# Performance work log

Hardware: AMD Instinct MI355X
Metric: run time of the kernel (lower is better)

Reference implementation:

```python
import jax, jax.numpy as jnp
import numpy as np

GAMMA = 2.0
CONTEXT_WINDOW = 100


def setup_inputs() -> dict:
    key = jax.random.key(0)
    k1, k2 = jax.random.split(key)
    B, S, C = 64, 131072, 3
    inputs = jax.random.normal(k1, (B, S, C), dtype=jnp.float32)
    targets = jax.random.randint(k2, (B, S), 0, C, dtype=jnp.int32)
    alpha = jnp.array([0.25, 1.0, 1.0], dtype=jnp.float32)
    return {"inputs": inputs, "targets": targets, "alpha": alpha}


def _window_mask(targets, window):
    # mask[b, i] = True iff any positive target within +/- window of i;
    # rows with no positives are fully True (matches torch loop semantics).
    B, S = targets.shape
    pos = targets > 0                                   # (B, S) bool
    cs = jnp.cumsum(pos.astype(jnp.int32), axis=1)      # inclusive prefix sums
    c = jnp.concatenate([jnp.zeros((B, 1), jnp.int32), cs], axis=1)  # (B, S+1)
    idx = jnp.arange(S)
    hi = jnp.minimum(idx + window + 1, S)               # exclusive end
    lo = jnp.maximum(idx - window, 0)                   # inclusive start
    count = c[:, hi] - c[:, lo]                         # positives in window
    mask = count > 0
    has_pos = pos.any(axis=1, keepdims=True)
    return jnp.where(has_pos, mask, True)


def reference(inputs, targets, alpha):
    # inputs: (B, S, C) logits; targets: (B, S) class indices
    mask = _window_mask(targets, CONTEXT_WINDOW)                     # (B, S)
    logp = jax.nn.log_softmax(inputs, axis=-1)                       # (B, S, C)
    ce = -jnp.take_along_axis(logp, targets[..., None].astype(jnp.int32), axis=-1)[..., 0]
    p_t = jnp.exp(-ce)
    focal = alpha[targets] * (1.0 - p_t) ** GAMMA * ce               # (B, S)
    m = mask.astype(inputs.dtype)
    # masked mean == mean over selected elements in the torch version
    return jnp.sum(focal * m) / jnp.sum(m)
```

## Files before the change

kernel.cpp:

```cpp
#include <hip/hip_runtime.h>

#define BB 64
#define SS 131072
#define WIN 100
#define TILE 2048
#define NTHREADS 256
#define NBLOCKS (BB * (SS / TILE))
#define EXT (TILE + 2*WIN)
#define NITER ((EXT + NTHREADS - 1) / NTHREADS)
#define NWORDS ((EXT + 63) / 64)

__global__ __launch_bounds__(NTHREADS) void focal_main(
    const float* __restrict__ inputs, const int* __restrict__ targets,
    const float* __restrict__ alpha, double* __restrict__ slots)
{
    __shared__ unsigned char sh_t[EXT];
    __shared__ unsigned long long wbits[NWORDS];
    __shared__ unsigned long long mbits[NWORDS];
    __shared__ double red[(NTHREADS/64) * 4];

    const int t = threadIdx.x;
    const int b = blockIdx.x >> 6;
    const int tile = blockIdx.x & 63;
    const int s0 = tile * TILE;
    const int ext_lo = (s0 - WIN > 0) ? (s0 - WIN) : 0;
    const int ext_hi = (s0 + TILE + WIN < SS) ? (s0 + TILE + WIN) : SS;
    const int ext_len = ext_hi - ext_lo;

    const float* inrow = inputs + (long)b * SS * 3;
    const int p0 = s0 + t * 4;
    const int p1 = s0 + (NTHREADS + t) * 4;
    const float4* ip0 = (const float4*)(inrow + (long)p0 * 3);
    const float4* ip1 = (const float4*)(inrow + (long)p1 * 3);
    const float4 q0 = ip0[0], q1 = ip0[1], q2 = ip0[2];
    const float4 q3 = ip1[0], q4 = ip1[1], q5 = ip1[2];

    const int* trow = targets + (long)b * SS;
    const int wave = t >> 6, lane = t & 63;
    const int tr_lo = s0 - ext_lo;
    int cnt_p = 0;
    #pragma unroll
    for (int it = 0; it < NITER; ++it) {
        const int k = it * NTHREADS + t;
        const int tv = (k < ext_len) ? trow[ext_lo + k] : 0;
        if (k < ext_len) sh_t[k] = (unsigned char)tv;
        const bool pos = (tv > 0);
        cnt_p += (pos && k >= tr_lo && k < tr_lo + TILE) ? 1 : 0;
        const unsigned long long bal = __ballot(pos);
        if (lane == 0) wbits[it * 4 + wave] = bal;
    }
    __syncthreads();

    if (wave == 0) {
        unsigned long long x = (lane < NWORDS) ? wbits[lane] : 0ULL;
        const int shifts[7] = {1, 2, 4, 8, 16, 32, 37};
        #pragma unroll
        for (int s_i = 0; s_i < 7; ++s_i) {
            const int s = shifts[s_i];
            unsigned long long up = __shfl_up(x, 1);
            if (lane == 0) up = 0ULL;
            unsigned long long dn = __shfl_down(x, 1);
            if (lane == 63) dn = 0ULL;
            x = x | (x << s) | (up >> (64 - s)) | (x >> s) | (dn << (64 - s));
        }
        if (lane < NWORDS) mbits[lane] = x;
    }
    __syncthreads();

    const float a0 = alpha[0], a1 = alpha[1], a2 = alpha[2];
    float fsum_m = 0.0f, fsum_a = 0.0f;
    int cnt_m = 0;

    const float xs[24] = {q0.x, q0.y, q0.z, q0.w, q1.x, q1.y, q1.z, q1.w,
                          q2.x, q2.y, q2.z, q2.w, q3.x, q3.y, q3.z, q3.w,
                          q4.x, q4.y, q4.z, q4.w, q5.x, q5.y, q5.z, q5.w};

    #pragma unroll
    for (int g = 0; g < 2; ++g) {
        const int p = (g == 0) ? p0 : p1;
        const int j0 = p - ext_lo;
        const unsigned long long mw = mbits[j0 >> 6];
        const unsigned int tpack = *(const unsigned int*)(sh_t + j0);
        #pragma unroll
        for (int j = 0; j < 4; ++j) {
            const float x0 = xs[g*12 + 3*j], x1 = xs[g*12 + 3*j + 1],
                        x2 = xs[g*12 + 3*j + 2];
            const int tv = (tpack >> (8 * j)) & 0xFF;
            const float mx = fmaxf(x0, fmaxf(x1, x2));
            const float e0 = __expf(x0 - mx), e1 = __expf(x1 - mx), e2 = __expf(x2 - mx);
            const float sum = e0 + e1 + e2;
            const float xt  = (tv == 0) ? x0 : ((tv == 1) ? x1 : x2);
            const float et  = (tv == 0) ? e0 : ((tv == 1) ? e1 : e2);
            const float ce  = __logf(sum) + (mx - xt);
            const float pt  = et * __frcp_rn(sum);
            const float w   = (tv == 0) ? a0 : ((tv == 1) ? a1 : a2);
            const float om  = 1.0f - pt;
            const float focal = w * om * om * ce;
            const bool  m   = (mw >> ((j0 & 63) + j)) & 1ULL;

            fsum_a += focal;
            fsum_m += m ? focal : 0.0f;
            cnt_m  += m ? 1 : 0;
        }
    }

    #pragma unroll
    for (int off = 32; off >= 1; off >>= 1) {
        fsum_m += __shfl_down(fsum_m, off);
        fsum_a += __shfl_down(fsum_a, off);
        cnt_m  += __shfl_down(cnt_m, off);
        cnt_p  += __shfl_down(cnt_p, off);
    }
    if (lane == 0) {
        red[wave*4]   = (double)fsum_m; red[wave*4+1] = (double)cnt_m;
        red[wave*4+2] = (double)fsum_a; red[wave*4+3] = (double)cnt_p;
    }
    __syncthreads();
    if (t == 0) {
        double sm = 0, sc = 0, sa = 0, sp = 0;
        #pragma unroll
        for (int w = 0; w < NTHREADS/64; ++w) {
            sm += red[w*4]; sc += red[w*4+1]; sa += red[w*4+2]; sp += red[w*4+3];
        }
        double* slot = slots + (long)blockIdx.x * 4;
        slot[0] = sm;
        slot[1] = sc;
        slot[2] = sa;
        slot[3] = sp;
    }
}

__global__ __launch_bounds__(NTHREADS) void focal_final(
    const double* __restrict__ slots, float* __restrict__ out)
{
    __shared__ double red[(NTHREADS/64) * 2];
    __shared__ double tot[2];
    const int t = threadIdx.x;
    const int wave = t >> 6, lane = t & 63;

    double sm = 0.0, sc = 0.0;
    for (int k = t; k < NBLOCKS; k += NTHREADS) {
        sm += slots[(long)k * 4 + 0];
        sc += slots[(long)k * 4 + 1];
    }
    #pragma unroll
    for (int off = 32; off >= 1; off >>= 1) {
        sm += __shfl_down(sm, off);
        sc += __shfl_down(sc, off);
    }
    if (lane == 0) { red[wave*2] = sm; red[wave*2+1] = sc; }
    __syncthreads();
    if (t == 0) {
        double a = 0, b = 0;
        #pragma unroll
        for (int w = 0; w < NTHREADS/64; ++w) { a += red[w*2]; b += red[w*2+1]; }
        tot[0] = a; tot[1] = b;
    }
    __syncthreads();

    double corr_s = 0.0, corr_c = 0.0;
    if (t < BB) {
        double row_sum = 0.0, row_pos = 0.0;
        for (int j = 0; j < 64; ++j) {
            const long blk = (long)t * 64 + j;
            row_sum += slots[blk * 4 + 2];
            row_pos += slots[blk * 4 + 3];
        }
        if (row_pos == 0.0) { corr_s = row_sum; corr_c = (double)SS; }
    }
    if (wave == 0) {
        #pragma unroll
        for (int off = 32; off >= 1; off >>= 1) {
            corr_s += __shfl_down(corr_s, off);
            corr_c += __shfl_down(corr_c, off);
        }
        if (t == 0) {
            const double total = tot[0] + corr_s;
            const double count = tot[1] + corr_c;
            out[0] = (float)(total / count);
        }
    }
}

extern "C" void kernel_launch(void* const* d_in, const int* in_sizes, int n_in,
                              void* d_out, int out_size, void* d_ws, size_t ws_size,
                              hipStream_t stream) {
    const float* inputs  = (const float*)d_in[0];
    const int*   targets = (const int*)d_in[1];
    const float* alpha   = (const float*)d_in[2];
    float* out = (float*)d_out;

    double* slots = (double*)d_ws;

    focal_main<<<NBLOCKS, NTHREADS, 0, stream>>>(inputs, targets, alpha, slots);
    focal_final<<<1, NTHREADS, 0, stream>>>(slots, out);
}
```

Before: 190.5 us.

## Double tile size, vectorize target staging, compute window mask via ctz/clz

Each block now covers 4096 positions instead of 2048, which halves the block count and the relative cost of re-reading the 100-element halo. Targets are loaded as int4 and packed into bytes in shared memory. The 64-bit positive-bit words are built from those bytes with bit tricks. The window dilation across 64-bit words now uses ctz/clz on the four neighbouring words instead of a seven-step shuffle dilation. Logits for the next group are prefetched into registers while the current group is computed, and launch bounds request 8 blocks per CU. Risks are higher register pressure and fewer blocks available for load balancing.

```diff
diff --git a/kernel.cpp b/kernel.cpp
--- a/kernel.cpp
+++ b/kernel.cpp
@@ -3,67 +3,99 @@
 #define BB 64
 #define SS 131072
 #define WIN 100
-#define TILE 2048
+#define TILE 4096
 #define NTHREADS 256
-#define NBLOCKS (BB * (SS / TILE))
+#define TILES_PER_ROW (SS / TILE)
+#define NBLOCKS (BB * TILES_PER_ROW)
 #define EXT (TILE + 2*WIN)
-#define NITER ((EXT + NTHREADS - 1) / NTHREADS)
 #define NWORDS ((EXT + 63) / 64)
-
-__global__ __launch_bounds__(NTHREADS) void focal_main(
+#define SH_BYTES (NWORDS * 64)
+#define K4TOT (SH_BYTES / 4)
+#define SROUNDS ((K4TOT + NTHREADS - 1) / NTHREADS)
+#define NGROUPS (TILE / (NTHREADS * 4))
+
+__global__ __launch_bounds__(NTHREADS, 8) void focal_main(
     const float* __restrict__ inputs, const int* __restrict__ targets,
     const float* __restrict__ alpha, double* __restrict__ slots)
 {
-    __shared__ unsigned char sh_t[EXT];
+    __shared__ __align__(16) unsigned char sh_t[SH_BYTES];
     __shared__ unsigned long long wbits[NWORDS];
     __shared__ unsigned long long mbits[NWORDS];
     __shared__ double red[(NTHREADS/64) * 4];
 
     const int t = threadIdx.x;
-    const int b = blockIdx.x >> 6;
-    const int tile = blockIdx.x & 63;
+    const int b = blockIdx.x / TILES_PER_ROW;
+    const int tile = blockIdx.x % TILES_PER_ROW;
     const int s0 = tile * TILE;
     const int ext_lo = (s0 - WIN > 0) ? (s0 - WIN) : 0;
     const int ext_hi = (s0 + TILE + WIN < SS) ? (s0 + TILE + WIN) : SS;
     const int ext_len = ext_hi - ext_lo;
+    const int tr_lo = s0 - ext_lo;
 
     const float* inrow = inputs + (long)b * SS * 3;
-    const int p0 = s0 + t * 4;
-    const int p1 = s0 + (NTHREADS + t) * 4;
-    const float4* ip0 = (const float4*)(inrow + (long)p0 * 3);
-    const float4* ip1 = (const float4*)(inrow + (long)p1 * 3);
-    const float4 q0 = ip0[0], q1 = ip0[1], q2 = ip0[2];
-    const float4 q3 = ip1[0], q4 = ip1[1], q5 = ip1[2];
+    const float4* gp0 = (const float4*)(inrow + (long)(s0 + t * 4) * 3);
+    float4 c0 = gp0[0], c1 = gp0[1], c2 = gp0[2];
 
     const int* trow = targets + (long)b * SS;
-    const int wave = t >> 6, lane = t & 63;
-    const int tr_lo = s0 - ext_lo;
+    #pragma unroll
+    for (int it = 0; it < SROUNDS; ++it) {
+        const int k4 = it * NTHREADS + t;
+        if (k4 < K4TOT) {
+            unsigned int pk = 0;
+            if (4 * k4 < ext_len) {
+                const int4 tv4 = *(const int4*)(trow + ext_lo + 4 * k4);
+                pk = (unsigned)(tv4.x & 3) | ((unsigned)(tv4.y & 3) << 8) |
+                     ((unsigned)(tv4.z & 3) << 16) | ((unsigned)(tv4.w & 3) << 24);
+            }
+            ((unsigned int*)sh_t)[k4] = pk;
+        }
+    }
+    __syncthreads();
+
     int cnt_p = 0;
-    #pragma unroll
-    for (int it = 0; it < NITER; ++it) {
-        const int k = it * NTHREADS + t;
-        const int tv = (k < ext_len) ? trow[ext_lo + k] : 0;
-        if (k < ext_len) sh_t[k] = (unsigned char)tv;
-        const bool pos = (tv > 0);
-        cnt_p += (pos && k >= tr_lo && k < tr_lo + TILE) ? 1 : 0;
-        const unsigned long long bal = __ballot(pos);
-        if (lane == 0) wbits[it * 4 + wave] = bal;
-    }
-    __syncthreads();
-
-    if (wave == 0) {
-        unsigned long long x = (lane < NWORDS) ? wbits[lane] : 0ULL;
-        const int shifts[7] = {1, 2, 4, 8, 16, 32, 37};
-        #pragma unroll
-        for (int s_i = 0; s_i < 7; ++s_i) {
-            const int s = shifts[s_i];
-            unsigned long long up = __shfl_up(x, 1);
-            if (lane == 0) up = 0ULL;
-            unsigned long long dn = __shfl_down(x, 1);
-            if (lane == 63) dn = 0ULL;
-            x = x | (x << s) | (up >> (64 - s)) | (x >> s) | (dn << (64 - s));
-        }
-        if (lane < NWORDS) mbits[lane] = x;
+    if (t < NWORDS) {
+        const uint4* qp = (const uint4*)(sh_t + (t << 6));
+        unsigned long long wv = 0;
+        #pragma unroll
+        for (int r = 0; r < 4; ++r) {
+            const uint4 u = qp[r];
+            unsigned int x, nz;
+            x = u.x; nz = (x | (x >> 1)) & 0x01010101u;
+            wv |= (unsigned long long)((nz * 0x01020408u) >> 24) << (r*16 + 0);
+            x = u.y; nz = (x | (x >> 1)) & 0x01010101u;
+            wv |= (unsigned long long)((nz * 0x01020408u) >> 24) << (r*16 + 4);
+            x = u.z; nz = (x | (x >> 1)) & 0x01010101u;
+            wv |= (unsigned long long)((nz * 0x01020408u) >> 24) << (r*16 + 8);
+            x = u.w; nz = (x | (x >> 1)) & 0x01010101u;
+            wv |= (unsigned long long)((nz * 0x01020408u) >> 24) << (r*16 + 12);
+        }
+        wbits[t] = wv;
+        int lo_bit = tr_lo - (t << 6);        if (lo_bit < 0) lo_bit = 0;
+        int hi_bit = tr_lo + TILE - (t << 6); if (hi_bit > 64) hi_bit = 64;
+        if (hi_bit > lo_bit) {
+            unsigned long long rm = (hi_bit >= 64) ? ~0ULL : ((1ULL << hi_bit) - 1);
+            rm &= (~0ULL << lo_bit);
+            cnt_p = __popcll(wv & rm);
+        }
+    }
+    __syncthreads();
+
+    if (t < NWORDS) {
+        const unsigned long long a = (t >= 2) ? wbits[t-2] : 0ULL;
+        const unsigned long long bw = (t >= 1) ? wbits[t-1] : 0ULL;
+        const unsigned long long c = wbits[t];
+        const unsigned long long d = (t+1 < NWORDS) ? wbits[t+1] : 0ULL;
+        const unsigned long long e = (t+2 < NWORDS) ? wbits[t+2] : 0ULL;
+        unsigned long long m = c ? ~0ULL : 0ULL;
+        if (d) { const int lo = __builtin_ctzll(d) - 36;
+                 m |= (lo <= 0) ? ~0ULL : (~0ULL << lo); }
+        if (e) { const int lo = __builtin_ctzll(e) + 28;
+                 if (lo <= 63) m |= (~0ULL << lo); }
+        if (bw) { const int hi = 63 - __builtin_clzll(bw) + 36;
+                  m |= (hi >= 63) ? ~0ULL : (~0ULL >> (63 - hi)); }
+        if (a) { const int hi = 63 - __builtin_clzll(a) - 28;
+                 if (hi >= 0) m |= (hi >= 63) ? ~0ULL : (~0ULL >> (63 - hi)); }
+        mbits[t] = m;
     }
     __syncthreads();
 
@@ -71,20 +103,23 @@
     float fsum_m = 0.0f, fsum_a = 0.0f;
     int cnt_m = 0;
 
-    const float xs[24] = {q0.x, q0.y, q0.z, q0.w, q1.x, q1.y, q1.z, q1.w,
-                          q2.x, q2.y, q2.z, q2.w, q3.x, q3.y, q3.z, q3.w,
-                          q4.x, q4.y, q4.z, q4.w, q5.x, q5.y, q5.z, q5.w};
-
-    #pragma unroll
-    for (int g = 0; g < 2; ++g) {
-        const int p = (g == 0) ? p0 : p1;
+    #pragma unroll
+    for (int g = 0; g < NGROUPS; ++g) {
+        float4 n0, n1, n2;
+        if (g + 1 < NGROUPS) {
+            const float4* gpn =
+                (const float4*)(inrow + (long)(s0 + ((g+1)*NTHREADS + t) * 4) * 3);
+            n0 = gpn[0]; n1 = gpn[1]; n2 = gpn[2];
+        }
+        const int p = s0 + (g*NTHREADS + t) * 4;
         const int j0 = p - ext_lo;
         const unsigned long long mw = mbits[j0 >> 6];
         const unsigned int tpack = *(const unsigned int*)(sh_t + j0);
+        const float xs[12] = {c0.x, c0.y, c0.z, c0.w, c1.x, c1.y, c1.z, c1.w,
+                              c2.x, c2.y, c2.z, c2.w};
         #pragma unroll
         for (int j = 0; j < 4; ++j) {
-            const float x0 = xs[g*12 + 3*j], x1 = xs[g*12 + 3*j + 1],
-                        x2 = xs[g*12 + 3*j + 2];
+            const float x0 = xs[3*j], x1 = xs[3*j+1], x2 = xs[3*j+2];
             const int tv = (tpack >> (8 * j)) & 0xFF;
             const float mx = fmaxf(x0, fmaxf(x1, x2));
             const float e0 = __expf(x0 - mx), e1 = __expf(x1 - mx), e2 = __expf(x2 - mx);
@@ -102,8 +137,10 @@
             fsum_m += m ? focal : 0.0f;
             cnt_m  += m ? 1 : 0;
         }
-    }
-
+        c0 = n0; c1 = n1; c2 = n2;
+    }
+
+    const int wave = t >> 6, lane = t & 63;
     #pragma unroll
     for (int off = 32; off >= 1; off >>= 1) {
         fsum_m += __shfl_down(fsum_m, off);
@@ -161,8 +198,8 @@
     double corr_s = 0.0, corr_c = 0.0;
     if (t < BB) {
         double row_sum = 0.0, row_pos = 0.0;
-        for (int j = 0; j < 64; ++j) {
-            const long blk = (long)t * 64 + j;
+        for (int j = 0; j < TILES_PER_ROW; ++j) {
+            const long blk = (long)t * TILES_PER_ROW + j;
             row_sum += slots[blk * 4 + 2];
             row_pos += slots[blk * 4 + 3];
         }
```

After: 178.9 us. 1.06x faster.

## Split window-mask construction into separate kernel and stream focal loss with prefetch

Applied to the files above, without the earlier changes.

Moves the window-mask computation into its own kernel that reads targets once, ballots them into bitwords and builds the mask from neighbouring words with ctz/clz, writing the mask bits and per-segment positive counts to workspace. The main kernel then processes larger tiles of 4096 with a register-prefetch loop over four groups, reading targets as int4 and mask words from global memory instead of re-reading halo targets into shared memory. The intent is to remove the redundant halo loads, the shared-memory staging and the two block-wide barriers from the main kernel. In exchange it adds a kernel launch and an extra pass over targets plus a mask write and read through global memory.

```diff
diff --git a/kernel.cpp b/kernel.cpp
--- a/kernel.cpp
+++ b/kernel.cpp
@@ -3,91 +3,109 @@
 #define BB 64
 #define SS 131072
 #define WIN 100
-#define TILE 2048
-#define NTHREADS 256
-#define NBLOCKS (BB * (SS / TILE))
-#define EXT (TILE + 2*WIN)
-#define NITER ((EXT + NTHREADS - 1) / NTHREADS)
-#define NWORDS ((EXT + 63) / 64)
-
-__global__ __launch_bounds__(NTHREADS) void focal_main(
+#define WPR (SS / 64)
+#define NWORDS_TOT (BB * WPR)
+
+#define AW 256
+#define ABLOCKS (NWORDS_TOT / AW)
+#define SEGS_PER_ROW (WPR / AW)
+
+#define TILE_B 4096
+#define TPR (SS / TILE_B)
+#define NB (BB * TPR)
+#define NGROUPS 4
+
+
+__global__ __launch_bounds__(256) void mask_build(
+    const int* __restrict__ targets, unsigned long long* __restrict__ mbits,
+    int* __restrict__ segpos)
+{
+    __shared__ unsigned long long sh[AW + 4];
+    __shared__ int pred[4];
+    const int t = threadIdx.x, wave = t >> 6, lane = t & 63;
+    const long wbase = (long)blockIdx.x * AW;
+    const long row   = wbase / WPR;
+    const long rlo   = row * WPR, rhi = rlo + WPR;
+
+    #pragma unroll
+    for (int it = 0; it < (AW + 4) / 4; ++it) {
+        const int idx = it * 4 + wave;
+        const long g = wbase - 2 + idx;
+        bool pos = false;
+        if (g >= rlo && g < rhi) pos = targets[g * 64 + lane] > 0;
+        const unsigned long long bal = __ballot(pos);
+        if (lane == 0) sh[idx] = bal;
+    }
+    __syncthreads();
+
+    const unsigned long long a  = sh[t];
+    const unsigned long long bw = sh[t + 1];
+    const unsigned long long c  = sh[t + 2];
+    const unsigned long long d  = sh[t + 3];
+    const unsigned long long e  = sh[t + 4];
+    unsigned long long m = c ? ~0ULL : 0ULL;
+    if (d)  { const int lo = __builtin_ctzll(d) - 36;
+              m |= (lo <= 0) ? ~0ULL : (~0ULL << lo); }
+    if (e)  { const int lo = __builtin_ctzll(e) + 28;
+              if (lo <= 63) m |= (~0ULL << lo); }
+    if (bw) { const int hi = 63 - __builtin_clzll(bw) + 36;
+              m |= (hi >= 63) ? ~0ULL : (~0ULL >> (63 - hi)); }
+    if (a)  { const int hi = 63 - __builtin_clzll(a) - 28;
+              if (hi >= 0) m |= (hi >= 63) ? ~0ULL : (~0ULL >> (63 - hi)); }
+    mbits[wbase + t] = m;
+
+    int pc = __popcll(c);
+    #pragma unroll
+    for (int off = 32; off >= 1; off >>= 1) pc += __shfl_down(pc, off);
+    if (lane == 0) pred[wave] = pc;
+    __syncthreads();
+    if (t == 0) segpos[blockIdx.x] = pred[0] + pred[1] + pred[2] + pred[3];
+}
+
+__global__ __launch_bounds__(256, 8) void focal_stream(
     const float* __restrict__ inputs, const int* __restrict__ targets,
+    const unsigned long long* __restrict__ mbits,
     const float* __restrict__ alpha, double* __restrict__ slots)
 {
-    __shared__ unsigned char sh_t[EXT];
-    __shared__ unsigned long long wbits[NWORDS];
-    __shared__ unsigned long long mbits[NWORDS];
-    __shared__ double red[(NTHREADS/64) * 4];
-
+    __shared__ double red[4 * 3];
     const int t = threadIdx.x;
-    const int b = blockIdx.x >> 6;
-    const int tile = blockIdx.x & 63;
-    const int s0 = tile * TILE;
-    const int ext_lo = (s0 - WIN > 0) ? (s0 - WIN) : 0;
-    const int ext_hi = (s0 + TILE + WIN < SS) ? (s0 + TILE + WIN) : SS;
-    const int ext_len = ext_hi - ext_lo;
-
+    const int b = blockIdx.x >> 5;
+    const int tile = blockIdx.x & 31;
+    const int s0 = tile * TILE_B;
     const float* inrow = inputs + (long)b * SS * 3;
-    const int p0 = s0 + t * 4;
-    const int p1 = s0 + (NTHREADS + t) * 4;
-    const float4* ip0 = (const float4*)(inrow + (long)p0 * 3);
-    const float4* ip1 = (const float4*)(inrow + (long)p1 * 3);
-    const float4 q0 = ip0[0], q1 = ip0[1], q2 = ip0[2];
-    const float4 q3 = ip1[0], q4 = ip1[1], q5 = ip1[2];
-
     const int* trow = targets + (long)b * SS;
-    const int wave = t >> 6, lane = t & 63;
-    const int tr_lo = s0 - ext_lo;
-    int cnt_p = 0;
-    #pragma unroll
-    for (int it = 0; it < NITER; ++it) {
-        const int k = it * NTHREADS + t;
-        const int tv = (k < ext_len) ? trow[ext_lo + k] : 0;
-        if (k < ext_len) sh_t[k] = (unsigned char)tv;
-        const bool pos = (tv > 0);
-        cnt_p += (pos && k >= tr_lo && k < tr_lo + TILE) ? 1 : 0;
-        const unsigned long long bal = __ballot(pos);
-        if (lane == 0) wbits[it * 4 + wave] = bal;
-    }
-    __syncthreads();
-
-    if (wave == 0) {
-        unsigned long long x = (lane < NWORDS) ? wbits[lane] : 0ULL;
-        const int shifts[7] = {1, 2, 4, 8, 16, 32, 37};
-        #pragma unroll
-        for (int s_i = 0; s_i < 7; ++s_i) {
-            const int s = shifts[s_i];
-            unsigned long long up = __shfl_up(x, 1);
-            if (lane == 0) up = 0ULL;
-            unsigned long long dn = __shfl_down(x, 1);
-            if (lane == 63) dn = 0ULL;
-            x = x | (x << s) | (up >> (64 - s)) | (x >> s) | (dn << (64 - s));
-        }
-        if (lane < NWORDS) mbits[lane] = x;
-    }
-    __syncthreads();
+    const unsigned long long* mrow = mbits + (long)b * WPR;
+
+    int p = s0 + t * 4;
+    const float4* ip = (const float4*)(inrow + (long)p * 3);
+    float4 c0 = ip[0], c1 = ip[1], c2 = ip[2];
+    int4 tv4 = *(const int4*)(trow + p);
+    unsigned long long mw = mrow[p >> 6];
 
     const float a0 = alpha[0], a1 = alpha[1], a2 = alpha[2];
-    float fsum_m = 0.0f, fsum_a = 0.0f;
-    int cnt_m = 0;
-
-    const float xs[24] = {q0.x, q0.y, q0.z, q0.w, q1.x, q1.y, q1.z, q1.w,
-                          q2.x, q2.y, q2.z, q2.w, q3.x, q3.y, q3.z, q3.w,
-                          q4.x, q4.y, q4.z, q4.w, q5.x, q5.y, q5.z, q5.w};
-
-    #pragma unroll
-    for (int g = 0; g < 2; ++g) {
-        const int p = (g == 0) ? p0 : p1;
-        const int j0 = p - ext_lo;
-        const unsigned long long mw = mbits[j0 >> 6];
-        const unsigned int tpack = *(const unsigned int*)(sh_t + j0);
+    float fm = 0.0f, fa = 0.0f;
+    int cm = 0;
+
+    #pragma unroll
+    for (int g = 0; g < NGROUPS; ++g) {
+        float4 n0, n1, n2; int4 ntv; unsigned long long nmw;
+        const int np = s0 + ((g + 1) * 256 + t) * 4;
+        if (g + 1 < NGROUPS) {
+            const float4* nip = (const float4*)(inrow + (long)np * 3);
+            n0 = nip[0]; n1 = nip[1]; n2 = nip[2];
+            ntv = *(const int4*)(trow + np);
+            nmw = mrow[np >> 6];
+        }
+        const float xs[12] = {c0.x, c0.y, c0.z, c0.w, c1.x, c1.y, c1.z, c1.w,
+                              c2.x, c2.y, c2.z, c2.w};
+        const int tvs[4] = {tv4.x, tv4.y, tv4.z, tv4.w};
+        const int bit0 = p & 63;
         #pragma unroll
         for (int j = 0; j < 4; ++j) {
-            const float x0 = xs[g*12 + 3*j], x1 = xs[g*12 + 3*j + 1],
-                        x2 = xs[g*12 + 3*j + 2];
-            const int tv = (tpack >> (8 * j)) & 0xFF;
-            const float mx = fmaxf(x0, fmaxf(x1, x2));
-            const float e0 = __expf(x0 - mx), e1 = __expf(x1 - mx), e2 = __expf(x2 - mx);
+            const float x0 = xs[3*j], x1 = xs[3*j+1], x2 = xs[3*j+2];
+            const int tv = tvs[j];
+            const float mx  = fmaxf(x0, fmaxf(x1, x2));
+            const float e0  = __expf(x0 - mx), e1 = __expf(x1 - mx), e2 = __expf(x2 - mx);
             const float sum = e0 + e1 + e2;
             const float xt  = (tv == 0) ? x0 : ((tv == 1) ? x1 : x2);
             const float et  = (tv == 0) ? e0 : ((tv == 1) ? e1 : e2);
@@ -96,52 +114,50 @@
             const float w   = (tv == 0) ? a0 : ((tv == 1) ? a1 : a2);
             const float om  = 1.0f - pt;
             const float focal = w * om * om * ce;
-            const bool  m   = (mw >> ((j0 & 63) + j)) & 1ULL;
-
-            fsum_a += focal;
-            fsum_m += m ? focal : 0.0f;
-            cnt_m  += m ? 1 : 0;
-        }
-    }
-
+            const bool  msk = (mw >> (bit0 + j)) & 1ULL;
+            fa += focal;
+            fm += msk ? focal : 0.0f;
+            cm += msk ? 1 : 0;
+        }
+        p = np;
+        c0 = n0; c1 = n1; c2 = n2; tv4 = ntv; mw = nmw;
+    }
+
+    const int wave = t >> 6, lane = t & 63;
     #pragma unroll
     for (int off = 32; off >= 1; off >>= 1) {
-        fsum_m += __shfl_down(fsum_m, off);
-        fsum_a += __shfl_down(fsum_a, off);
-        cnt_m  += __shfl_down(cnt_m, off);
-        cnt_p  += __shfl_down(cnt_p, off);
+        fm += __shfl_down(fm, off);
+        fa += __shfl_down(fa, off);
+        cm += __shfl_down(cm, off);
     }
     if (lane == 0) {
-        red[wave*4]   = (double)fsum_m; red[wave*4+1] = (double)cnt_m;
-        red[wave*4+2] = (double)fsum_a; red[wave*4+3] = (double)cnt_p;
+        red[wave*3] = (double)fm; red[wave*3+1] = (double)cm; red[wave*3+2] = (double)fa;
     }
     __syncthreads();
     if (t == 0) {
-        double sm = 0, sc = 0, sa = 0, sp = 0;
-        #pragma unroll
-        for (int w = 0; w < NTHREADS/64; ++w) {
-            sm += red[w*4]; sc += red[w*4+1]; sa += red[w*4+2]; sp += red[w*4+3];
-        }
-        double* slot = slots + (long)blockIdx.x * 4;
-        slot[0] = sm;
-        slot[1] = sc;
-        slot[2] = sa;
-        slot[3] = sp;
-    }
-}
-
-__global__ __launch_bounds__(NTHREADS) void focal_final(
-    const double* __restrict__ slots, float* __restrict__ out)
+        double sm = 0, sc = 0, sa = 0;
+        #pragma unroll
+        for (int w = 0; w < 4; ++w) {
+            sm += red[w*3]; sc += red[w*3+1]; sa += red[w*3+2];
+        }
+        double* slot = slots + (long)blockIdx.x * 3;
+        slot[0] = sm; slot[1] = sc; slot[2] = sa;
+    }
+}
+
+__global__ __launch_bounds__(256) void focal_final(
+    const double* __restrict__ slots, const int* __restrict__ segpos,
+    float* __restrict__ out)
 {
-    __shared__ double red[(NTHREADS/64) * 2];
+    __shared__ double red[4 * 2];
     __shared__ double tot[2];
     const int t = threadIdx.x;
     const int wave = t >> 6, lane = t & 63;
 
     double sm = 0.0, sc = 0.0;
-    for (int k = t; k < NBLOCKS; k += NTHREADS) {
-        sm += slots[(long)k * 4 + 0];
-        sc += slots[(long)k * 4 + 1];
+    for (int k = t; k < NB; k += 256) {
+        sm += slots[(long)k * 3 + 0];
+        sc += slots[(long)k * 3 + 1];
     }
     #pragma unroll
     for (int off = 32; off >= 1; off >>= 1) {
@@ -153,20 +169,21 @@
     if (t == 0) {
         double a = 0, b = 0;
         #pragma unroll
-        for (int w = 0; w < NTHREADS/64; ++w) { a += red[w*2]; b += red[w*2+1]; }
+        for (int w = 0; w < 4; ++w) { a += red[w*2]; b += red[w*2+1]; }
         tot[0] = a; tot[1] = b;
     }
     __syncthreads();
 
     double corr_s = 0.0, corr_c = 0.0;
     if (t < BB) {
-        double row_sum = 0.0, row_pos = 0.0;
-        for (int j = 0; j < 64; ++j) {
-            const long blk = (long)t * 64 + j;
-            row_sum += slots[blk * 4 + 2];
-            row_pos += slots[blk * 4 + 3];
-        }
-        if (row_pos == 0.0) { corr_s = row_sum; corr_c = (double)SS; }
+        int rp = 0;
+        for (int j = 0; j < SEGS_PER_ROW; ++j) rp += segpos[t * SEGS_PER_ROW + j];
+        if (rp == 0) {
+            double row_sum = 0.0;
+            for (int j = 0; j < TPR; ++j)
+                row_sum += slots[((long)t * TPR + j) * 3 + 2];
+            corr_s = row_sum; corr_c = (double)SS;
+        }
     }
     if (wave == 0) {
         #pragma unroll
@@ -174,11 +191,7 @@
             corr_s += __shfl_down(corr_s, off);
             corr_c += __shfl_down(corr_c, off);
         }
-        if (t == 0) {
-            const double total = tot[0] + corr_s;
-            const double count = tot[1] + corr_c;
-            out[0] = (float)(total / count);
-        }
+        if (t == 0) out[0] = (float)((tot[0] + corr_s) / (tot[1] + corr_c));
     }
 }
 
@@ -190,8 +203,11 @@
     const float* alpha   = (const float*)d_in[2];
     float* out = (float*)d_out;
 
-    double* slots = (double*)d_ws;
-
-    focal_main<<<NBLOCKS, NTHREADS, 0, stream>>>(inputs, targets, alpha, slots);
-    focal_final<<<1, NTHREADS, 0, stream>>>(slots, out);
-}
+    unsigned long long* mbits = (unsigned long long*)d_ws;
+    int* segpos = (int*)((char*)d_ws + NWORDS_TOT * 8);
+    double* slots = (double*)((char*)d_ws + NWORDS_TOT * 8 + 2048);
+
+    mask_build<<<ABLOCKS, 256, 0, stream>>>(targets, mbits, segpos);
+    focal_stream<<<NB, 256, 0, stream>>>(inputs, targets, mbits, alpha, slots);
+    focal_final<<<1, 256, 0, stream>>>(slots, segpos, out);
+}
```

After: 205.4 us. 7.8% more time.
